# Kernel tuning notes

Measured on AMD Instinct MI355X. Metric: run time of the kernel, lower is better.

The kernel has to match this reference:

```python
import jax, jax.numpy as jnp
import numpy as np

NUM_LAYERS = 3

def setup_inputs() -> dict:
    key = jax.random.key(0)
    k1, k2, k3, k4 = jax.random.split(key, 4)
    N, D, E = 100000, 128, 3200000
    x = jax.random.normal(k1, (N, D), dtype=jnp.float32)
    edge_row = jax.random.randint(k2, (E,), 0, N, dtype=jnp.int64 if jax.config.jax_enable_x64 else jnp.int32)
    edge_col = jax.random.randint(k3, (E,), 0, N, dtype=jnp.int64 if jax.config.jax_enable_x64 else jnp.int32)
    # normalized-adjacency-like positive values
    edge_val = jax.random.uniform(k4, (E,), dtype=jnp.float32)
    return {"x": x, "edge_row": edge_row, "edge_col": edge_col, "edge_val": edge_val}

def _spmm(edge_row, edge_col, edge_val, emb, num_nodes):
    # out[r] += val * emb[c]  -- sparse adjacency @ emb
    msgs = edge_val[:, None] * emb[edge_col]          # [E, D] gather + scale
    return jax.ops.segment_sum(msgs, edge_row, num_segments=num_nodes)

def reference(x, edge_row, edge_col, edge_val):
    N = x.shape[0]
    emb = x
    acc = x  # running sum over layer embeddings (layer 0 included)
    for _ in range(NUM_LAYERS):
        emb = _spmm(edge_row, edge_col, edge_val, emb, N)
        acc = acc + emb
    # mean over (num_layers + 1) stacked embeddings, without materializing the stack
    return acc / jnp.float32(NUM_LAYERS + 1)
```

## Files before the change

kernel.cpp:

```cpp
#include <hip/hip_runtime.h>

#define DIMS 128
#define RPB 64
#define CAP 3072
#define NBK_MAX 1600
#define NBINS 1024

typedef _Float16 half_t;
typedef _Float16 half2_t __attribute__((ext_vector_type(2)));

static __device__ __forceinline__ unsigned halfbits(float v) {
    half_t h = (half_t)v;
    unsigned short us;
    __builtin_memcpy(&us, &h, 2);
    return (unsigned)us;
}

__global__ void cvt_kernel(const float* __restrict__ src, half_t* __restrict__ dst, int n2) {
    int i = blockIdx.x * blockDim.x + threadIdx.x;
    if (i >= n2) return;
    float2 v = reinterpret_cast<const float2*>(src)[i];
    half2_t h;
    h.x = (half_t)v.x;
    h.y = (half_t)v.y;
    reinterpret_cast<half2_t*>(&dst[0])[i] = h;
}

__global__ __launch_bounds__(256) void binA_kernel(
    const int* __restrict__ row, const int* __restrict__ col,
    const float* __restrict__ val, int E, int nbk,
    int* __restrict__ fill, int2* __restrict__ staged) {
    __shared__ int cnt[NBK_MAX];
    __shared__ int base[NBK_MAX];
    const int t = threadIdx.x;
    const int tile0 = blockIdx.x * 8192;
    for (int j = t; j < nbk; j += 256) cnt[j] = 0;
    __syncthreads();
    for (int k = 0; k < 8; ++k) {
        int e = tile0 + (k * 256 + t) * 4;
        if (e + 3 < E) {
            int4 r4 = *reinterpret_cast<const int4*>(&row[e]);
            atomicAdd(&cnt[r4.x >> 6], 1);
            atomicAdd(&cnt[r4.y >> 6], 1);
            atomicAdd(&cnt[r4.z >> 6], 1);
            atomicAdd(&cnt[r4.w >> 6], 1);
        } else {
            for (int j = e; j < E; ++j) atomicAdd(&cnt[row[j] >> 6], 1);
        }
    }
    __syncthreads();
    for (int j = t; j < nbk; j += 256) {
        int c = cnt[j];
        base[j] = c ? atomicAdd(&fill[j], c) : 0;
        cnt[j] = 0;
    }
    __syncthreads();
    for (int k = 0; k < 8; ++k) {
        int e = tile0 + (k * 256 + t) * 4;
        int n = (e + 3 < E) ? 4 : max(0, E - e);
        if (n == 4) {
            int4 r4 = *reinterpret_cast<const int4*>(&row[e]);
            int4 c4 = *reinterpret_cast<const int4*>(&col[e]);
            float4 v4 = *reinterpret_cast<const float4*>(&val[e]);
            int rr[4] = {r4.x, r4.y, r4.z, r4.w};
            int cc[4] = {c4.x, c4.y, c4.z, c4.w};
            float vv[4] = {v4.x, v4.y, v4.z, v4.w};
#pragma unroll
            for (int j = 0; j < 4; ++j) {
                int b = rr[j] >> 6;
                int p = base[b] + atomicAdd(&cnt[b], 1);
                if (p < CAP) {
                    unsigned hb = halfbits(vv[j]);
                    int2 pk;
                    pk.x = (int)(((unsigned)(rr[j] & 63) << 26) | ((unsigned)cc[j] << 8));
                    pk.y = (int)((hb << 16) | hb);
                    staged[(size_t)b * CAP + p] = pk;
                }
            }
        } else {
            for (int j = e; j < e + n; ++j) {
                int r = row[j];
                int b = r >> 6;
                int p = base[b] + atomicAdd(&cnt[b], 1);
                if (p < CAP) {
                    unsigned hb = halfbits(val[j]);
                    int2 pk;
                    pk.x = (int)(((unsigned)(r & 63) << 26) | ((unsigned)col[j] << 8));
                    pk.y = (int)((hb << 16) | hb);
                    staged[(size_t)b * CAP + p] = pk;
                }
            }
        }
    }
}

__global__ __launch_bounds__(512) void sort_bucket(
    const int* __restrict__ fill, int2* __restrict__ staged,
    int* __restrict__ rowinfo, int N) {
    __shared__ int2 buf[CAP];
    __shared__ int2 outb[CAP];
    __shared__ int cur[NBINS];
    __shared__ int wsum[8];
    const int b = blockIdx.x;
    const int t = threadIdx.x;
    const int w = t >> 6, lane = t & 63;
    const int cnt = min(fill[b], CAP);
    int2* gb = staged + (size_t)b * CAP;

    cur[2 * t] = 0;
    cur[2 * t + 1] = 0;
    for (int i = t; i < cnt; i += 512) buf[i] = gb[i];
    __syncthreads();
    for (int i = t; i < cnt; i += 512) {
        unsigned k = (unsigned)buf[i].x;
        int key = (int)((k >> 26) << 4) | (int)((k >> 21) & 0xF);
        atomicAdd(&cur[key], 1);
    }
    __syncthreads();
    int h0 = cur[2 * t], h1 = cur[2 * t + 1];
    int s = h0 + h1;
    int v = s;
    for (int d = 1; d < 64; d <<= 1) {
        int u = __shfl_up(v, d, 64);
        if (lane >= d) v += u;
    }
    if (lane == 63) wsum[w] = v;
    __syncthreads();
    if (t < 8) {
        int ws = wsum[t];
        int vv = ws;
        for (int d = 1; d < 8; d <<= 1) {
            int u = __shfl_up(vv, d, 64);
            if (t >= d) vv += u;
        }
        wsum[t] = vv - ws;
    }
    __syncthreads();
    int excl = wsum[w] + (v - s);
    cur[2 * t] = excl;
    cur[2 * t + 1] = excl + h0;
    __syncthreads();
    if (t < RPB) {
        int start = cur[t * 16];
        int end = (t == RPB - 1) ? cnt : cur[t * 16 + 16];
        int r = b * RPB + t;
        if (r < N) rowinfo[r] = (start << 16) | end;
    }
    __syncthreads();
    for (int i = t; i < cnt; i += 512) {
        int2 pk = buf[i];
        unsigned k = (unsigned)pk.x;
        int key = (int)((k >> 26) << 4) | (int)((k >> 21) & 0xF);
        int p = atomicAdd(&cur[key], 1);
        outb[p] = pk;
    }
    __syncthreads();
    for (int i = t; i < cnt; i += 512) gb[i] = outb[i];
}

template <int MODE>
__global__ __launch_bounds__(256) void spmm_kernel(
    const half_t* __restrict__ emb_in, const int* __restrict__ rowinfo,
    const int2* __restrict__ staged, int N,
    half_t* __restrict__ emb_out, half_t* __restrict__ acc_h,
    float* __restrict__ out) {
    int r = (blockIdx.x * blockDim.x + threadIdx.x) >> 6;
    int lane = threadIdx.x & 63;
    if (r >= N) return;
    int info = rowinfo[r];
    int start = info >> 16;
    int end = info & 0xFFFF;
    const int2* eb = staged + (size_t)(r >> 6) * CAP;
    const char* tbl = reinterpret_cast<const char*>(emb_in);
    const unsigned lane4 = (unsigned)lane << 2;

    half2_t acc[8];
#pragma unroll
    for (int k = 0; k < 8; ++k) acc[k] = (half2_t)0;

    for (int base = start; base < end; base += 64) {
        const int cnt = min(64, end - base);
        int2 myE = make_int2(0, 0);
        if (base + lane < end) myE = eb[base + lane];

        int k = 0;
        for (; k + 7 < cnt; k += 8) {
            int ex[8], ey[8];
#pragma unroll
            for (int j = 0; j < 8; ++j) {
                ex[j] = __shfl(myE.x, k + j, 64);
                ey[j] = __shfl(myE.y, k + j, 64);
            }
            half2_t tv[8];
#pragma unroll
            for (int j = 0; j < 8; ++j) {
                unsigned voff = (((unsigned)ex[j]) & 0x03FFFF00u) + lane4;
                tv[j] = *reinterpret_cast<const half2_t*>(tbl + voff);
            }
#pragma unroll
            for (int j = 0; j < 8; ++j) {
                half2_t vv = __builtin_bit_cast(half2_t, ey[j]);
                acc[j] = tv[j] * vv + acc[j];
            }
        }
        for (; k < cnt; ++k) {
            int ex = __shfl(myE.x, k, 64);
            int ey = __shfl(myE.y, k, 64);
            unsigned voff = (((unsigned)ex) & 0x03FFFF00u) + lane4;
            half2_t tvs = *reinterpret_cast<const half2_t*>(tbl + voff);
            half2_t vv = __builtin_bit_cast(half2_t, ey);
            acc[0] = tvs * vv + acc[0];
        }
    }
    half2_t a01 = acc[0] + acc[1], a23 = acc[2] + acc[3];
    half2_t a45 = acc[4] + acc[5], a67 = acc[6] + acc[7];
    half2_t a = (a01 + a23) + (a45 + a67);

    size_t o = (size_t)r * DIMS + 2 * lane;
    if (MODE == 0 || MODE == 1) {
        *reinterpret_cast<half2_t*>(&emb_out[o]) = a;
    }
    if (MODE == 0) {
        half2_t xv = *reinterpret_cast<const half2_t*>(&emb_in[o]);
        *reinterpret_cast<half2_t*>(&acc_h[o]) = xv + a;
    } else if (MODE == 1) {
        half2_t cv = *reinterpret_cast<half2_t*>(&acc_h[o]);
        *reinterpret_cast<half2_t*>(&acc_h[o]) = cv + a;
    } else {
        half2_t cv = *reinterpret_cast<half2_t*>(&acc_h[o]);
        *reinterpret_cast<float2*>(&out[o]) =
            make_float2(((float)cv.x + (float)a.x) * 0.25f,
                        ((float)cv.y + (float)a.y) * 0.25f);
    }
}


extern "C" void kernel_launch(void* const* d_in, const int* in_sizes, int n_in,
                              void* d_out, int out_size, void* d_ws, size_t ws_size,
                              hipStream_t stream) {
    const float* x = (const float*)d_in[0];
    const int* erow = (const int*)d_in[1];
    const int* ecol = (const int*)d_in[2];
    const float* eval = (const float*)d_in[3];
    const int N = in_sizes[0] / DIMS;
    const int E = in_sizes[1];
    float* out = (float*)d_out;
    const int nbk = (N + RPB - 1) / RPB;

    char* ws = (char*)d_ws;
    size_t off = 0;
    auto carve = [&](size_t bytes) {
        void* p = ws + off;
        off = (off + bytes + 255) & ~(size_t)255;
        return p;
    };
    half_t* xh = (half_t*)carve((size_t)N * DIMS * sizeof(half_t));
    half_t* embB1 = (half_t*)carve((size_t)N * DIMS * sizeof(half_t));
    half_t* acc_h = (half_t*)carve((size_t)N * DIMS * sizeof(half_t));
    int2* staged = (int2*)carve((size_t)nbk * CAP * sizeof(int2));
    int* fill = (int*)carve((size_t)nbk * sizeof(int));
    int* rowinfo = (int*)carve((size_t)N * sizeof(int));
    (void)ws_size;

    hipMemsetAsync(fill, 0, (size_t)nbk * sizeof(int), stream);
    const int n2 = N * DIMS / 2;
    cvt_kernel<<<(n2 + 255) / 256, 256, 0, stream>>>(x, xh, n2);
    binA_kernel<<<(E + 8191) / 8192, 256, 0, stream>>>(erow, ecol, eval, E, nbk, fill, staged);
    sort_bucket<<<nbk, 512, 0, stream>>>(fill, staged, rowinfo, N);

    const int spmm_blocks = (N + 3) / 4;
    spmm_kernel<0><<<spmm_blocks, 256, 0, stream>>>(xh, rowinfo, staged, N, embB1, acc_h, out);
    spmm_kernel<1><<<spmm_blocks, 256, 0, stream>>>(embB1, rowinfo, staged, N, xh, acc_h, out);
    spmm_kernel<2><<<spmm_blocks, 256, 0, stream>>>(xh, rowinfo, staged, N, embB1, acc_h, out);
}
```

Before: 541.3 us.

## Replace bin+sort preprocessing with global histogram scan scatter; use 16B gathers in SpMM

The two-pass bin-then-sort-in-shared-memory preprocessing is replaced by three simple passes. A global atomic histogram keyed on (row, col>>13) is followed by a per-bucket prefix scan that writes rowinfo, then a scatter that places edges using atomics on the scanned offsets. The histogram lives in the reused embB1 buffer. Separately, the SpMM kernel now has each 16-lane group fetch a whole 256-byte row with 16-byte loads, processing four edges per wave step and reducing across groups with shuffles. This cuts the number of load instructions per edge and removes the shared-memory sort, in exchange for more global atomics and a cross-lane reduction.

Measured after the change: 1.763 ms. +225.7%, slower.

```diff
diff --git a/kernel.cpp b/kernel.cpp
--- a/kernel.cpp
+++ b/kernel.cpp
@@ -3,7 +3,6 @@
 #define DIMS 128
 #define RPB 64
 #define CAP 3072
-#define NBK_MAX 1600
 #define NBINS 1024
 
 typedef _Float16 half_t;
@@ -15,6 +14,8 @@
     __builtin_memcpy(&us, &h, 2);
     return (unsigned)us;
 }
+static __device__ __forceinline__ half2_t h2(int b) { return __builtin_bit_cast(half2_t, b); }
+static __device__ __forceinline__ int ih(half2_t h) { return __builtin_bit_cast(int, h); }
 
 __global__ void cvt_kernel(const float* __restrict__ src, half_t* __restrict__ dst, int n2) {
     int i = blockIdx.x * blockDim.x + threadIdx.x;
@@ -26,136 +27,98 @@
     reinterpret_cast<half2_t*>(&dst[0])[i] = h;
 }
 
-__global__ __launch_bounds__(256) void binA_kernel(
-    const int* __restrict__ row, const int* __restrict__ col,
-    const float* __restrict__ val, int E, int nbk,
-    int* __restrict__ fill, int2* __restrict__ staged) {
-    __shared__ int cnt[NBK_MAX];
-    __shared__ int base[NBK_MAX];
-    const int t = threadIdx.x;
-    const int tile0 = blockIdx.x * 8192;
-    for (int j = t; j < nbk; j += 256) cnt[j] = 0;
-    __syncthreads();
-    for (int k = 0; k < 8; ++k) {
-        int e = tile0 + (k * 256 + t) * 4;
-        if (e + 3 < E) {
-            int4 r4 = *reinterpret_cast<const int4*>(&row[e]);
-            atomicAdd(&cnt[r4.x >> 6], 1);
-            atomicAdd(&cnt[r4.y >> 6], 1);
-            atomicAdd(&cnt[r4.z >> 6], 1);
-            atomicAdd(&cnt[r4.w >> 6], 1);
-        } else {
-            for (int j = e; j < E; ++j) atomicAdd(&cnt[row[j] >> 6], 1);
-        }
-    }
-    __syncthreads();
-    for (int j = t; j < nbk; j += 256) {
-        int c = cnt[j];
-        base[j] = c ? atomicAdd(&fill[j], c) : 0;
-        cnt[j] = 0;
-    }
-    __syncthreads();
-    for (int k = 0; k < 8; ++k) {
-        int e = tile0 + (k * 256 + t) * 4;
-        int n = (e + 3 < E) ? 4 : max(0, E - e);
-        if (n == 4) {
-            int4 r4 = *reinterpret_cast<const int4*>(&row[e]);
-            int4 c4 = *reinterpret_cast<const int4*>(&col[e]);
-            float4 v4 = *reinterpret_cast<const float4*>(&val[e]);
-            int rr[4] = {r4.x, r4.y, r4.z, r4.w};
-            int cc[4] = {c4.x, c4.y, c4.z, c4.w};
-            float vv[4] = {v4.x, v4.y, v4.z, v4.w};
-#pragma unroll
-            for (int j = 0; j < 4; ++j) {
-                int b = rr[j] >> 6;
-                int p = base[b] + atomicAdd(&cnt[b], 1);
-                if (p < CAP) {
-                    unsigned hb = halfbits(vv[j]);
-                    int2 pk;
-                    pk.x = (int)(((unsigned)(rr[j] & 63) << 26) | ((unsigned)cc[j] << 8));
-                    pk.y = (int)((hb << 16) | hb);
-                    staged[(size_t)b * CAP + p] = pk;
-                }
-            }
-        } else {
-            for (int j = e; j < e + n; ++j) {
-                int r = row[j];
-                int b = r >> 6;
-                int p = base[b] + atomicAdd(&cnt[b], 1);
-                if (p < CAP) {
-                    unsigned hb = halfbits(val[j]);
-                    int2 pk;
-                    pk.x = (int)(((unsigned)(r & 63) << 26) | ((unsigned)col[j] << 8));
-                    pk.y = (int)((hb << 16) | hb);
-                    staged[(size_t)b * CAP + p] = pk;
-                }
-            }
-        }
-    }
-}
-
-__global__ __launch_bounds__(512) void sort_bucket(
-    const int* __restrict__ fill, int2* __restrict__ staged,
-    int* __restrict__ rowinfo, int N) {
-    __shared__ int2 buf[CAP];
-    __shared__ int2 outb[CAP];
-    __shared__ int cur[NBINS];
-    __shared__ int wsum[8];
+__global__ __launch_bounds__(256) void hist_kernel(
+    const int* __restrict__ row, const int* __restrict__ col, int E,
+    int* __restrict__ hist) {
+    int e = (blockIdx.x * 256 + threadIdx.x) * 4;
+    if (e + 3 < E) {
+        int4 r4 = *reinterpret_cast<const int4*>(&row[e]);
+        int4 c4 = *reinterpret_cast<const int4*>(&col[e]);
+        atomicAdd(&hist[(r4.x << 4) + (c4.x >> 13)], 1);
+        atomicAdd(&hist[(r4.y << 4) + (c4.y >> 13)], 1);
+        atomicAdd(&hist[(r4.z << 4) + (c4.z >> 13)], 1);
+        atomicAdd(&hist[(r4.w << 4) + (c4.w >> 13)], 1);
+    } else {
+        for (int j = e; j < E; ++j)
+            atomicAdd(&hist[(row[j] << 4) + (col[j] >> 13)], 1);
+    }
+}
+
+__global__ __launch_bounds__(256) void scan_kernel(
+    int* __restrict__ hist, int* __restrict__ rowinfo, int N) {
+    __shared__ int pos[NBINS + 1];
+    __shared__ int wsum[4];
     const int b = blockIdx.x;
     const int t = threadIdx.x;
-    const int w = t >> 6, lane = t & 63;
-    const int cnt = min(fill[b], CAP);
-    int2* gb = staged + (size_t)b * CAP;
-
-    cur[2 * t] = 0;
-    cur[2 * t + 1] = 0;
-    for (int i = t; i < cnt; i += 512) buf[i] = gb[i];
-    __syncthreads();
-    for (int i = t; i < cnt; i += 512) {
-        unsigned k = (unsigned)buf[i].x;
-        int key = (int)((k >> 26) << 4) | (int)((k >> 21) & 0xF);
-        atomicAdd(&cur[key], 1);
-    }
-    __syncthreads();
-    int h0 = cur[2 * t], h1 = cur[2 * t + 1];
-    int s = h0 + h1;
+    const int lane = t & 63, w = t >> 6;
+    int* hb = hist + (size_t)b * NBINS;
+    int4 h = *reinterpret_cast<const int4*>(&hb[4 * t]);
+    const int s = h.x + h.y + h.z + h.w;
     int v = s;
+#pragma unroll
     for (int d = 1; d < 64; d <<= 1) {
         int u = __shfl_up(v, d, 64);
         if (lane >= d) v += u;
     }
     if (lane == 63) wsum[w] = v;
     __syncthreads();
-    if (t < 8) {
-        int ws = wsum[t];
-        int vv = ws;
-        for (int d = 1; d < 8; d <<= 1) {
-            int u = __shfl_up(vv, d, 64);
-            if (t >= d) vv += u;
-        }
-        wsum[t] = vv - ws;
-    }
-    __syncthreads();
-    int excl = wsum[w] + (v - s);
-    cur[2 * t] = excl;
-    cur[2 * t + 1] = excl + h0;
+    int wbase = 0;
+    if (w > 0) wbase += wsum[0];
+    if (w > 1) wbase += wsum[1];
+    if (w > 2) wbase += wsum[2];
+    const int e0 = wbase + v - s;
+    const int e1 = e0 + h.x, e2 = e1 + h.y, e3 = e2 + h.z;
+    pos[4 * t] = e0;
+    pos[4 * t + 1] = e1;
+    pos[4 * t + 2] = e2;
+    pos[4 * t + 3] = e3;
+    if (t == 255) pos[NBINS] = e3 + h.w;
+    *reinterpret_cast<int4*>(&hb[4 * t]) = make_int4(e0, e1, e2, e3);
     __syncthreads();
     if (t < RPB) {
-        int start = cur[t * 16];
-        int end = (t == RPB - 1) ? cnt : cur[t * 16 + 16];
-        int r = b * RPB + t;
-        if (r < N) rowinfo[r] = (start << 16) | end;
-    }
-    __syncthreads();
-    for (int i = t; i < cnt; i += 512) {
-        int2 pk = buf[i];
-        unsigned k = (unsigned)pk.x;
-        int key = (int)((k >> 26) << 4) | (int)((k >> 21) & 0xF);
-        int p = atomicAdd(&cur[key], 1);
-        outb[p] = pk;
-    }
-    __syncthreads();
-    for (int i = t; i < cnt; i += 512) gb[i] = outb[i];
+        const int rstart = min(pos[t * 16], CAP);
+        const int rend = min(pos[t * 16 + 16], CAP);
+        const int rr = b * RPB + t;
+        if (rr < N) rowinfo[rr] = (rstart << 16) | rend;
+    }
+}
+
+__global__ __launch_bounds__(256) void scatter_kernel(
+    const int* __restrict__ row, const int* __restrict__ col,
+    const float* __restrict__ val, int E,
+    int* __restrict__ hist, int2* __restrict__ staged) {
+    int e = (blockIdx.x * 256 + threadIdx.x) * 4;
+    if (e + 3 < E) {
+        int4 r4 = *reinterpret_cast<const int4*>(&row[e]);
+        int4 c4 = *reinterpret_cast<const int4*>(&col[e]);
+        float4 v4 = *reinterpret_cast<const float4*>(&val[e]);
+        int rr[4] = {r4.x, r4.y, r4.z, r4.w};
+        int cc[4] = {c4.x, c4.y, c4.z, c4.w};
+        float vv[4] = {v4.x, v4.y, v4.z, v4.w};
+#pragma unroll
+        for (int j = 0; j < 4; ++j) {
+            int p = atomicAdd(&hist[(rr[j] << 4) + (cc[j] >> 13)], 1);
+            if (p < CAP) {
+                unsigned hb = halfbits(vv[j]);
+                int2 pk;
+                pk.x = (int)((unsigned)cc[j] << 8);
+                pk.y = (int)((hb << 16) | hb);
+                staged[(size_t)(rr[j] >> 6) * CAP + p] = pk;
+            }
+        }
+    } else {
+        for (int j = e; j < E; ++j) {
+            int r = row[j], c = col[j];
+            int p = atomicAdd(&hist[(r << 4) + (c >> 13)], 1);
+            if (p < CAP) {
+                unsigned hb = halfbits(val[j]);
+                int2 pk;
+                pk.x = (int)((unsigned)c << 8);
+                pk.y = (int)((hb << 16) | hb);
+                staged[(size_t)(r >> 6) * CAP + p] = pk;
+            }
+        }
+    }
 }
 
 template <int MODE>
@@ -164,19 +127,22 @@
     const int2* __restrict__ staged, int N,
     half_t* __restrict__ emb_out, half_t* __restrict__ acc_h,
     float* __restrict__ out) {
-    int r = (blockIdx.x * blockDim.x + threadIdx.x) >> 6;
-    int lane = threadIdx.x & 63;
+    const int r = (blockIdx.x * blockDim.x + threadIdx.x) >> 6;
+    const int lane = threadIdx.x & 63;
     if (r >= N) return;
-    int info = rowinfo[r];
-    int start = info >> 16;
-    int end = info & 0xFFFF;
+    const int info = rowinfo[r];
+    const int start = info >> 16;
+    const int end = info & 0xFFFF;
     const int2* eb = staged + (size_t)(r >> 6) * CAP;
     const char* tbl = reinterpret_cast<const char*>(emb_in);
-    const unsigned lane4 = (unsigned)lane << 2;
-
-    half2_t acc[8];
-#pragma unroll
-    for (int k = 0; k < 8; ++k) acc[k] = (half2_t)0;
+    const int g = lane >> 4;
+    const unsigned q16 = (unsigned)(lane & 15) << 4;
+
+    half2_t acc[4][4];
+#pragma unroll
+    for (int u = 0; u < 4; ++u)
+#pragma unroll
+        for (int s = 0; s < 4; ++s) acc[u][s] = (half2_t)0;
 
     for (int base = start; base < end; base += 64) {
         const int cnt = min(64, end - base);
@@ -184,53 +150,85 @@
         if (base + lane < end) myE = eb[base + lane];
 
         int k = 0;
-        for (; k + 7 < cnt; k += 8) {
-            int ex[8], ey[8];
-#pragma unroll
-            for (int j = 0; j < 8; ++j) {
-                ex[j] = __shfl(myE.x, k + j, 64);
-                ey[j] = __shfl(myE.y, k + j, 64);
-            }
-            half2_t tv[8];
-#pragma unroll
-            for (int j = 0; j < 8; ++j) {
-                unsigned voff = (((unsigned)ex[j]) & 0x03FFFF00u) + lane4;
-                tv[j] = *reinterpret_cast<const half2_t*>(tbl + voff);
-            }
-#pragma unroll
-            for (int j = 0; j < 8; ++j) {
-                half2_t vv = __builtin_bit_cast(half2_t, ey[j]);
-                acc[j] = tv[j] * vv + acc[j];
-            }
-        }
-        for (; k < cnt; ++k) {
-            int ex = __shfl(myE.x, k, 64);
-            int ey = __shfl(myE.y, k, 64);
-            unsigned voff = (((unsigned)ex) & 0x03FFFF00u) + lane4;
-            half2_t tvs = *reinterpret_cast<const half2_t*>(tbl + voff);
-            half2_t vv = __builtin_bit_cast(half2_t, ey);
-            acc[0] = tvs * vv + acc[0];
-        }
-    }
-    half2_t a01 = acc[0] + acc[1], a23 = acc[2] + acc[3];
-    half2_t a45 = acc[4] + acc[5], a67 = acc[6] + acc[7];
-    half2_t a = (a01 + a23) + (a45 + a67);
-
-    size_t o = (size_t)r * DIMS + 2 * lane;
-    if (MODE == 0 || MODE == 1) {
-        *reinterpret_cast<half2_t*>(&emb_out[o]) = a;
-    }
-    if (MODE == 0) {
-        half2_t xv = *reinterpret_cast<const half2_t*>(&emb_in[o]);
-        *reinterpret_cast<half2_t*>(&acc_h[o]) = xv + a;
-    } else if (MODE == 1) {
-        half2_t cv = *reinterpret_cast<half2_t*>(&acc_h[o]);
-        *reinterpret_cast<half2_t*>(&acc_h[o]) = cv + a;
-    } else {
-        half2_t cv = *reinterpret_cast<half2_t*>(&acc_h[o]);
-        *reinterpret_cast<float2*>(&out[o]) =
-            make_float2(((float)cv.x + (float)a.x) * 0.25f,
-                        ((float)cv.y + (float)a.y) * 0.25f);
+        for (; k + 16 <= cnt; k += 16) {
+            int ex[4], ey[4];
+#pragma unroll
+            for (int u = 0; u < 4; ++u) {
+                ex[u] = __shfl(myE.x, k + 4 * u + g, 64);
+                ey[u] = __shfl(myE.y, k + 4 * u + g, 64);
+            }
+            int4 tv[4];
+#pragma unroll
+            for (int u = 0; u < 4; ++u) {
+                unsigned voff = ((unsigned)ex[u] & 0x03FFFF00u) + q16;
+                tv[u] = *reinterpret_cast<const int4*>(tbl + voff);
+            }
+#pragma unroll
+            for (int u = 0; u < 4; ++u) {
+                half2_t vv = h2(ey[u]);
+                acc[u][0] = h2(tv[u].x) * vv + acc[u][0];
+                acc[u][1] = h2(tv[u].y) * vv + acc[u][1];
+                acc[u][2] = h2(tv[u].z) * vv + acc[u][2];
+                acc[u][3] = h2(tv[u].w) * vv + acc[u][3];
+            }
+        }
+        for (; k < cnt; k += 4) {
+            const int idx = k + g;
+            const int cl = min(idx, cnt - 1);
+            int ex = __shfl(myE.x, cl, 64);
+            int ey = __shfl(myE.y, cl, 64);
+            if (idx >= cnt) ey = 0;
+            unsigned voff = ((unsigned)ex & 0x03FFFF00u) + q16;
+            int4 t4 = *reinterpret_cast<const int4*>(tbl + voff);
+            half2_t vv = h2(ey);
+            const int u = (k >> 2) & 3;
+            acc[u][0] = h2(t4.x) * vv + acc[u][0];
+            acc[u][1] = h2(t4.y) * vv + acc[u][1];
+            acc[u][2] = h2(t4.z) * vv + acc[u][2];
+            acc[u][3] = h2(t4.w) * vv + acc[u][3];
+        }
+    }
+
+    half2_t a0 = (acc[0][0] + acc[1][0]) + (acc[2][0] + acc[3][0]);
+    half2_t a1 = (acc[0][1] + acc[1][1]) + (acc[2][1] + acc[3][1]);
+    half2_t a2 = (acc[0][2] + acc[1][2]) + (acc[2][2] + acc[3][2]);
+    half2_t a3 = (acc[0][3] + acc[1][3]) + (acc[2][3] + acc[3][3]);
+#pragma unroll
+    for (int off = 16; off < 64; off <<= 1) {
+        a0 = a0 + h2(__shfl_xor(ih(a0), off, 64));
+        a1 = a1 + h2(__shfl_xor(ih(a1), off, 64));
+        a2 = a2 + h2(__shfl_xor(ih(a2), off, 64));
+        a3 = a3 + h2(__shfl_xor(ih(a3), off, 64));
+    }
+
+    if (lane < 16) {
+        const size_t o = (size_t)r * DIMS + ((size_t)lane << 3);
+        if (MODE == 0 || MODE == 1) {
+            *reinterpret_cast<int4*>(&emb_out[o]) = make_int4(ih(a0), ih(a1), ih(a2), ih(a3));
+        }
+        if (MODE == 0) {
+            int4 xv = *reinterpret_cast<const int4*>(&emb_in[o]);
+            *reinterpret_cast<int4*>(&acc_h[o]) = make_int4(
+                ih(h2(xv.x) + a0), ih(h2(xv.y) + a1), ih(h2(xv.z) + a2), ih(h2(xv.w) + a3));
+        } else if (MODE == 1) {
+            int4 cv = *reinterpret_cast<const int4*>(&acc_h[o]);
+            *reinterpret_cast<int4*>(&acc_h[o]) = make_int4(
+                ih(h2(cv.x) + a0), ih(h2(cv.y) + a1), ih(h2(cv.z) + a2), ih(h2(cv.w) + a3));
+        } else {
+            int4 cv = *reinterpret_cast<const int4*>(&acc_h[o]);
+            half2_t c0 = h2(cv.x), c1 = h2(cv.y), c2 = h2(cv.z), c3 = h2(cv.w);
+            float4 f0 = make_float4(((float)c0.x + (float)a0.x) * 0.25f,
+                                    ((float)c0.y + (float)a0.y) * 0.25f,
+                                    ((float)c1.x + (float)a1.x) * 0.25f,
+                                    ((float)c1.y + (float)a1.y) * 0.25f);
+            float4 f1 = make_float4(((float)c2.x + (float)a2.x) * 0.25f,
+                                    ((float)c2.y + (float)a2.y) * 0.25f,
+                                    ((float)c3.x + (float)a3.x) * 0.25f,
+                                    ((float)c3.y + (float)a3.y) * 0.25f);
+            float4* po = reinterpret_cast<float4*>(&out[o]);
+            po[0] = f0;
+            po[1] = f1;
+        }
     }
 }
 
@@ -258,15 +256,17 @@
     half_t* embB1 = (half_t*)carve((size_t)N * DIMS * sizeof(half_t));
     half_t* acc_h = (half_t*)carve((size_t)N * DIMS * sizeof(half_t));
     int2* staged = (int2*)carve((size_t)nbk * CAP * sizeof(int2));
-    int* fill = (int*)carve((size_t)nbk * sizeof(int));
     int* rowinfo = (int*)carve((size_t)N * sizeof(int));
+    int* hist = (int*)embB1;
     (void)ws_size;
 
-    hipMemsetAsync(fill, 0, (size_t)nbk * sizeof(int), stream);
+    hipMemsetAsync(hist, 0, (size_t)nbk * NBINS * sizeof(int), stream);
     const int n2 = N * DIMS / 2;
     cvt_kernel<<<(n2 + 255) / 256, 256, 0, stream>>>(x, xh, n2);
-    binA_kernel<<<(E + 8191) / 8192, 256, 0, stream>>>(erow, ecol, eval, E, nbk, fill, staged);
-    sort_bucket<<<nbk, 512, 0, stream>>>(fill, staged, rowinfo, N);
+    const int eblocks = (E + 1023) / 1024;
+    hist_kernel<<<eblocks, 256, 0, stream>>>(erow, ecol, E, hist);
+    scan_kernel<<<nbk, 256, 0, stream>>>(hist, rowinfo, N);
+    scatter_kernel<<<eblocks, 256, 0, stream>>>(erow, ecol, eval, E, hist, staged);
 
     const int spmm_blocks = (N + 3) / 4;
     spmm_kernel<0><<<spmm_blocks, 256, 0, stream>>>(xh, rowinfo, staged, N, embB1, acc_h, out);
```
